# Performance work log

Measured on AMD Instinct MI355X. Metric: run time of the kernel, lower is better.

The kernel has to match this reference:

```python
import jax, jax.numpy as jnp
import numpy as np

NUM_LAYER = 3
LEAKY = 0.8
RES = 0.8  # residual scale in convolution


def spmm(row, col, val, x, n):
    # sparse (n x n) COO @ dense (n x d)
    return jax.ops.segment_sum(val[:, None] * x[col], row, num_segments=n)


def convolution(emb, row, col, val):
    n = emb.shape[0]
    all_e = emb
    acc = emb  # layer-0 term
    for _ in range(NUM_LAYER):
        all_e = spmm(row, col, val, all_e, n) + RES * all_e
        acc = acc + all_e
    return acc / (NUM_LAYER + 1)


def setup_inputs() -> dict:
    key = jax.random.key(0)
    ks = jax.random.split(key, 32)
    B, NU, NQ, NC, DE, DF = 16384, 50000, 20000, 512, 64, 128
    EU, EQ, EK = 1600000, 640000, 16384
    inp = {}
    inp['user_id'] = jax.random.randint(ks[0], (B,), 0, NU)
    inp['question_id'] = jax.random.randint(ks[1], (B,), 0, NQ)
    inp['q_table'] = (jax.random.uniform(ks[2], (NQ, NC)) < 0.05).astype(jnp.float32)
    inp['u_row'] = jax.random.randint(ks[3], (EU,), 0, NU)
    inp['u_col'] = jax.random.randint(ks[4], (EU,), 0, NU)
    inp['u_val'] = jax.random.uniform(ks[5], (EU,)) / 32.0
    inp['e_row'] = jax.random.randint(ks[6], (EQ,), 0, NQ)
    inp['e_col'] = jax.random.randint(ks[7], (EQ,), 0, NQ)
    inp['e_val'] = jax.random.uniform(ks[8], (EQ,)) / 32.0
    inp['k_row'] = jax.random.randint(ks[9], (EK,), 0, NC)
    inp['k_col'] = jax.random.randint(ks[10], (EK,), 0, NC)
    inp['k_val'] = jax.random.uniform(ks[11], (EK,)) / 32.0
    inp['student_emb'] = jax.random.normal(ks[12], (NU, DE)) * 0.1
    inp['exercise_emb'] = jax.random.normal(ks[13], (NQ, DE)) * 0.1
    inp['knowledge_emb'] = jax.random.normal(ks[14], (NC, DE)) * 0.1
    inp['W_s'] = jax.random.normal(ks[15], (DE, DF)) * 0.1
    inp['b_s'] = jnp.zeros((DF,))
    inp['W_e'] = jax.random.normal(ks[16], (DE, DF)) * 0.1
    inp['b_e'] = jnp.zeros((DF,))
    inp['W_k'] = jax.random.normal(ks[17], (DE, DF)) * 0.1
    inp['b_k'] = jnp.zeros((DF,))
    inp['W_d'] = jax.random.normal(ks[18], (DE, 1)) * 0.1
    inp['b_d'] = jnp.zeros((1,))
    inp['M1_w'] = jax.random.normal(ks[19], (NC, 512)) * 0.05
    inp['M1_b'] = jnp.zeros((512,))
    inp['M2_w'] = jax.random.normal(ks[20], (512, 256)) * 0.05
    inp['M2_b'] = jnp.zeros((256,))
    inp['M3_w'] = jax.random.normal(ks[21], (256, 128)) * 0.05
    inp['M3_b'] = jnp.zeros((128,))
    inp['M4_w'] = jax.random.normal(ks[22], (128, 1)) * 0.05
    inp['M4_b'] = jnp.zeros((1,))
    return inp


def reference(user_id, question_id, q_table,
              u_row, u_col, u_val, e_row, e_col, e_val, k_row, k_col, k_val,
              student_emb, exercise_emb, knowledge_emb,
              W_s, b_s, W_e, b_e, W_k, b_k, W_d, b_d,
              M1_w, M1_b, M2_w, M2_b, M3_w, M3_b, M4_w, M4_b):
    cs = convolution(student_emb, u_row, u_col, u_val)    # [NU, DE]
    ce = convolution(exercise_emb, e_row, e_col, e_val)   # [NQ, DE]
    ck = convolution(knowledge_emb, k_row, k_col, k_val)  # [NC, DE]
    bs = cs[user_id]        # [B, DE]
    be = ce[question_id]    # [B, DE]
    sf = jax.nn.leaky_relu(bs @ W_s + b_s, LEAKY)   # [B, DF]
    ef = jax.nn.leaky_relu(be @ W_e + b_e, LEAKY)   # [B, DF]
    kf = jax.nn.leaky_relu(ck @ W_k + b_k, LEAKY)   # [NC, DF]
    disc = jax.nn.sigmoid(be @ W_d + b_d)           # [B, 1]
    state = disc * ((sf - ef) @ kf.T) * q_table[question_id]  # [B, NC]
    h = jnp.tanh(state @ M1_w + M1_b)
    h = jnp.tanh(h @ M2_w + M2_b)
    h = jnp.tanh(h @ M3_w + M3_b)
    return jax.nn.sigmoid(h @ M4_w + M4_b).reshape(-1)  # [B]
```

## Files before the change

### kernel.cpp

```cpp
#include <hip/hip_runtime.h>
#include <hip/hip_bf16.h>
#include <math.h>

#define RESF 0.8f
#define LEAKYF 0.8f
#define BWSH 6
#define BWID 64
#define BSTRIDE 2432
#define BINCH 5120
#define BINR 5

typedef __attribute__((ext_vector_type(8))) short bs8;
typedef __attribute__((ext_vector_type(4))) float f32x4;

__device__ __forceinline__ void gload16(const void* g, void* l) {
  __builtin_amdgcn_global_load_lds((const __attribute__((address_space(1))) void*)g,
                                   (__attribute__((address_space(3))) void*)l, 16, 0, 0);
}

__device__ __forceinline__ float tanh_fast(float x) {
  float t = __expf(2.f * x);
  return 1.f - 2.f * __builtin_amdgcn_rcpf(1.f + t);
}
__device__ __forceinline__ float sigmoid_fast(float x) {
  return __builtin_amdgcn_rcpf(1.f + __expf(-x));
}
__device__ __forceinline__ float bf2f(ushort u) {
  return __uint_as_float((unsigned)u << 16);
}
__device__ __forceinline__ ushort f2bf(float a) {
  __hip_bfloat16 h = __float2bfloat16(a);
  return *(ushort*)&h;
}

__device__ __forceinline__ int edge_row(int e, const int* __restrict__ rU, const int* __restrict__ rE,
                                        const int* __restrict__ rK, int EU, int EQ, int NU, int NQ) {
  if (e < EU) return rU[e];
  if ((e -= EU) < EQ) return NU + rE[e];
  e -= EQ;
  return NU + NQ + rK[e];
}

__device__ __forceinline__ void edge_full(int e,
    const int* __restrict__ rU, const int* __restrict__ cU, const float* __restrict__ vU,
    const int* __restrict__ rE, const int* __restrict__ cE, const float* __restrict__ vE,
    const int* __restrict__ rK, const int* __restrict__ cK, const float* __restrict__ vK,
    int EU, int EQ, int NU, int NQ, int& grow, int& gcol, float& val) {
  if (e < EU) { grow = rU[e]; gcol = cU[e]; val = vU[e]; return; }
  if ((e -= EU) < EQ) { grow = NU + rE[e]; gcol = NU + cE[e]; val = vE[e]; return; }
  e -= EQ;
  grow = NU + NQ + rK[e]; gcol = NU + NQ + cK[e]; val = vK[e];
}

__global__ __launch_bounds__(256) void k_setup(int* __restrict__ gcur, int* __restrict__ flags,
                                               int* __restrict__ nneed, int nbuck, int N_tot) {
  int i = blockIdx.x * 256 + threadIdx.x;
  if (i < nbuck) gcur[i] = i * BSTRIDE;
  if (i < N_tot) flags[i] = 0;
  if (i == 0) nneed[0] = 0;
}

__global__ __launch_bounds__(1024) void k_bin(
    const int* __restrict__ rU, const int* __restrict__ cU, const float* __restrict__ vU,
    const int* __restrict__ rE, const int* __restrict__ cE, const float* __restrict__ vE,
    const int* __restrict__ rK, const int* __restrict__ cK, const float* __restrict__ vK,
    int* __restrict__ gcur, int2* __restrict__ tmp,
    int EU, int EQ, int EK, int NU, int NQ, int nbuck) {
  extern __shared__ int l[];
  int metaN = (2 * nbuck + 3) & ~3;
  int* cnt = l;
  int* dstb = l + nbuck;
  int2* spk = (int2*)(l + metaN);
  ushort* sbk = (ushort*)(spk + BINCH);
  __shared__ int wsum[16];

  int t = threadIdx.x;
  int lane = t & 63, wid = t >> 6;
  for (int i = t; i < nbuck; i += 1024) cnt[i] = 0;
  __syncthreads();

  int E = EU + EQ + EK;
  int lo = blockIdx.x * BINCH;
  int hi = lo + BINCH < E ? lo + BINCH : E;
  int m = hi - lo;

  int2 pk[BINR];
  int bk[BINR];
#pragma unroll
  for (int k = 0; k < BINR; ++k) {
    int e = lo + t + k * 1024;
    bk[k] = -1;
    if (e < hi) {
      int grow, gcol;
      float val;
      edge_full(e, rU, cU, vU, rE, cE, vE, rK, cK, vK, EU, EQ, NU, NQ, grow, gcol, val);
      pk[k].x = ((grow & (BWID - 1)) << 26) | gcol;
      pk[k].y = __float_as_int(val);
      int b = grow >> BWSH;
      bk[k] = b;
      atomicAdd(&cnt[b], 1);
    }
  }
  __syncthreads();

  int carry = 0;
  for (int base = 0; base < nbuck; base += 1024) {
    int i = base + t;
    int x = (i < nbuck) ? cnt[i] : 0;
    int v = x;
#pragma unroll
    for (int d = 1; d < 64; d <<= 1) {
      int y = __shfl_up(v, d);
      if (lane >= d) v += y;
    }
    if (lane == 63) wsum[wid] = v;
    __syncthreads();
    if (t < 16) {
      int w = wsum[t];
#pragma unroll
      for (int d = 1; d < 16; d <<= 1) {
        int y = __shfl_up(w, d);
        if (t >= d) w += y;
      }
      wsum[t] = w;
    }
    __syncthreads();
    int excl = carry + ((wid > 0) ? wsum[wid - 1] : 0) + v - x;
    if (i < nbuck) {
      int gb = x ? atomicAdd(&gcur[i], x) : 0;
      dstb[i] = gb - excl;
      cnt[i] = excl;
    }
    carry += wsum[15];
    __syncthreads();
  }

#pragma unroll
  for (int k = 0; k < BINR; ++k) {
    if (bk[k] >= 0) {
      int p = atomicAdd(&cnt[bk[k]], 1);
      spk[p] = pk[k];
      sbk[p] = (ushort)bk[k];
    }
  }
  __syncthreads();

  for (int i = t; i < m; i += 1024) {
    int b = sbk[i];
    tmp[dstb[b] + i] = spk[i];
  }
}

__global__ __launch_bounds__(1024) void k_scan2(const int* __restrict__ gcur, int* __restrict__ boff, int n) {
  __shared__ int s[16];
  int tid = threadIdx.x;
  int lane = tid & 63, wid = tid >> 6;
  int carry = 0;
  for (int base = 0; base < n; base += 1024) {
    int i = base + tid;
    int x = (i < n) ? (gcur[i] - i * BSTRIDE) : 0;
    int v = x;
#pragma unroll
    for (int d = 1; d < 64; d <<= 1) {
      int t = __shfl_up(v, d);
      if (lane >= d) v += t;
    }
    if (lane == 63) s[wid] = v;
    __syncthreads();
    if (tid < 16) {
      int w = s[tid];
#pragma unroll
      for (int d = 1; d < 16; d <<= 1) {
        int t = __shfl_up(w, d);
        if (tid >= d) w += t;
      }
      s[tid] = w;
    }
    __syncthreads();
    int wofs = (wid > 0) ? s[wid - 1] : 0;
    int total = s[15];
    if (i < n) boff[i] = carry + wofs + v - x;
    carry += total;
    __syncthreads();
  }
  if (tid == 0) boff[n] = carry;
}

__global__ __launch_bounds__(256) void k_sort(const int2* __restrict__ tmp, int2* __restrict__ sorted,
                                              const int* __restrict__ gcur, const int* __restrict__ boff,
                                              int* __restrict__ roff, int N_tot, int E_tot) {
  __shared__ int2 sedge[BSTRIDE];
  __shared__ int cnt[BWID];
  __shared__ int cur[BWID];
  int b = blockIdx.x, t = threadIdx.x;
  int beg = b * BSTRIDE, end = gcur[b];
  int m = end - beg;
  if (m > BSTRIDE) m = BSTRIDE;
  int dst = boff[b];
  if (t < BWID) cnt[t] = 0;
  __syncthreads();
  for (int i = t; i < m; i += 256) {
    int2 pe = tmp[beg + i];
    sedge[i] = pe;
    atomicAdd(&cnt[((unsigned)pe.x) >> 26], 1);
  }
  __syncthreads();
  if (t < BWID) {
    int x = cnt[t];
    int v = x;
#pragma unroll
    for (int d = 1; d < 64; d <<= 1) {
      int y = __shfl_up(v, d);
      if (t >= d) v += y;
    }
    cur[t] = v - x;
    int r = (b << BWSH) + t;
    if (r < N_tot) roff[r] = dst + v - x;
  }
  __syncthreads();
  for (int i = t; i < m; i += 256) {
    int2 pe = sedge[i];
    int rl = ((unsigned)pe.x) >> 26;
    int rank = atomicAdd(&cur[rl], 1);
    sorted[dst + rank] = pe;
  }
  if (b == 0 && t == 0) roff[N_tot] = E_tot;
}

__global__ __launch_bounds__(256) void k_flag(const int* __restrict__ user_id,
                                              const int* __restrict__ question_id,
                                              int* __restrict__ flags, int B, int NU) {
  int i = blockIdx.x * 256 + threadIdx.x;
  if (i < B) {
    flags[user_id[i]] = 1;
    flags[NU + question_id[i]] = 1;
  }
}

__global__ __launch_bounds__(256) void k_compact(const int* __restrict__ flags, int* __restrict__ list,
                                                 int* __restrict__ nneed, int N_tot, int NUQ) {
  int i = blockIdx.x * 256 + threadIdx.x;
  if (i >= N_tot) return;
  if (flags[i] || i >= NUQ) {
    int p = atomicAdd(nneed, 1);
    list[p] = i;
  }
}

__global__ __launch_bounds__(256) void k_init3(ushort* __restrict__ lay0,
                                               const float* __restrict__ embU,
                                               const float* __restrict__ embE,
                                               const float* __restrict__ embK,
                                               int n4U, int n4E, int n4K) {
  int n4 = n4U + n4E + n4K;
  int stride = gridDim.x * 256;
  ushort4* c4 = (ushort4*)lay0;
  for (int i = blockIdx.x * 256 + threadIdx.x; i < n4; i += stride) {
    const float4* src;
    int j = i;
    if (j < n4U) src = (const float4*)embU;
    else if ((j -= n4U) < n4E) src = (const float4*)embE;
    else { j -= n4E; src = (const float4*)embK; }
    float4 v = src[j];
    ushort4 u;
    u.x = f2bf(v.x); u.y = f2bf(v.y); u.z = f2bf(v.z); u.w = f2bf(v.w);
    c4[i] = u;
  }
}

__device__ __forceinline__ void spmm_core(const ushort* __restrict__ curb,
                                          const int2* __restrict__ edges,
                                          int beg, int end, int li, int eh,
                                          float& a0, float& a1, float& a2, float& a3) {
  int lane = (eh << 4) | li;
  for (int base = beg; base < end; base += 64) {
    int rem = end - base;
    int m = rem < 64 ? rem : 64;
    int c = 0, vi = 0;
    if (lane < m) {
      int2 pe = edges[base + lane];
      c = pe.x & 0x3FFFFFF;
      vi = pe.y;
    }
    for (int j = 0; j * 4 < m; j += 4) {
      int s0 = (j + 0) * 4 + eh, s1 = (j + 1) * 4 + eh;
      int s2 = (j + 2) * 4 + eh, s3 = (j + 3) * 4 + eh;
      int cc0 = __shfl(c, s0), cc1 = __shfl(c, s1), cc2 = __shfl(c, s2), cc3 = __shfl(c, s3);
      float vf0 = __int_as_float(__shfl(vi, s0));
      float vf1 = __int_as_float(__shfl(vi, s1));
      float vf2 = __int_as_float(__shfl(vi, s2));
      float vf3 = __int_as_float(__shfl(vi, s3));
      uint2 x0 = *(const uint2*)&curb[(size_t)cc0 * 64 + 4 * li];
      uint2 x1 = *(const uint2*)&curb[(size_t)cc1 * 64 + 4 * li];
      uint2 x2 = *(const uint2*)&curb[(size_t)cc2 * 64 + 4 * li];
      uint2 x3 = *(const uint2*)&curb[(size_t)cc3 * 64 + 4 * li];
      a0 = fmaf(vf0, __uint_as_float(x0.x << 16), a0);
      a1 = fmaf(vf0, __uint_as_float(x0.x & 0xffff0000u), a1);
      a2 = fmaf(vf0, __uint_as_float(x0.y << 16), a2);
      a3 = fmaf(vf0, __uint_as_float(x0.y & 0xffff0000u), a3);
      a0 = fmaf(vf1, __uint_as_float(x1.x << 16), a0);
      a1 = fmaf(vf1, __uint_as_float(x1.x & 0xffff0000u), a1);
      a2 = fmaf(vf1, __uint_as_float(x1.y << 16), a2);
      a3 = fmaf(vf1, __uint_as_float(x1.y & 0xffff0000u), a3);
      a0 = fmaf(vf2, __uint_as_float(x2.x << 16), a0);
      a1 = fmaf(vf2, __uint_as_float(x2.x & 0xffff0000u), a1);
      a2 = fmaf(vf2, __uint_as_float(x2.y << 16), a2);
      a3 = fmaf(vf2, __uint_as_float(x2.y & 0xffff0000u), a3);
      a0 = fmaf(vf3, __uint_as_float(x3.x << 16), a0);
      a1 = fmaf(vf3, __uint_as_float(x3.x & 0xffff0000u), a1);
      a2 = fmaf(vf3, __uint_as_float(x3.y << 16), a2);
      a3 = fmaf(vf3, __uint_as_float(x3.y & 0xffff0000u), a3);
    }
  }
  a0 += __shfl_xor(a0, 16); a0 += __shfl_xor(a0, 32);
  a1 += __shfl_xor(a1, 16); a1 += __shfl_xor(a1, 32);
  a2 += __shfl_xor(a2, 16); a2 += __shfl_xor(a2, 32);
  a3 += __shfl_xor(a3, 16); a3 += __shfl_xor(a3, 32);
}

__global__ __launch_bounds__(256) void k_spmm2(const ushort* __restrict__ curb,
                                               ushort* __restrict__ nxtb,
                                               const int* __restrict__ off,
                                               const int2* __restrict__ edges, int n) {
  int r = blockIdx.x * 4 + (threadIdx.x >> 6);
  if (r >= n) return;
  int lane = threadIdx.x & 63;
  int li = lane & 15, eh = lane >> 4;
  int beg = off[r], end = off[r + 1];
  float a0 = 0.f, a1 = 0.f, a2 = 0.f, a3 = 0.f;
  spmm_core(curb, edges, beg, end, li, eh, a0, a1, a2, a3);
  if (eh == 0) {
    size_t gi = (size_t)r * 64 + 4 * li;
    uint2 cv = *(const uint2*)&curb[gi];
    a0 = fmaf(RESF, __uint_as_float(cv.x << 16), a0);
    a1 = fmaf(RESF, __uint_as_float(cv.x & 0xffff0000u), a1);
    a2 = fmaf(RESF, __uint_as_float(cv.y << 16), a2);
    a3 = fmaf(RESF, __uint_as_float(cv.y & 0xffff0000u), a3);
    uint2 o;
    o.x = ((unsigned)f2bf(a1) << 16) | f2bf(a0);
    o.y = ((unsigned)f2bf(a3) << 16) | f2bf(a2);
    *(uint2*)&nxtb[gi] = o;
  }
}

__global__ __launch_bounds__(256) void k_spmm3(const ushort* __restrict__ curb,
                                               const ushort* __restrict__ lay1,
                                               const float* __restrict__ embU,
                                               const float* __restrict__ embE,
                                               const float* __restrict__ embK,
                                               float* __restrict__ acc,
                                               const int* __restrict__ off,
                                               const int2* __restrict__ edges,
                                               const int* __restrict__ list,
                                               const int* __restrict__ nneed,
                                               int NU, int NQ) {
  int idx = blockIdx.x * 4 + (threadIdx.x >> 6);
  if (idx >= *nneed) return;
  int r = list[idx];
  int lane = threadIdx.x & 63;
  int li = lane & 15, eh = lane >> 4;
  int beg = off[r], end = off[r + 1];
  float a0 = 0.f, a1 = 0.f, a2 = 0.f, a3 = 0.f;
  spmm_core(curb, edges, beg, end, li, eh, a0, a1, a2, a3);
  if (eh == 0) {
    size_t gi = (size_t)r * 64 + 4 * li;
    const float* ep;
    if (r < NU) ep = embU + gi;
    else if (r < NU + NQ) ep = embE + (gi - (size_t)NU * 64);
    else ep = embK + (gi - (size_t)(NU + NQ) * 64);
    float4 e = *(const float4*)ep;
    uint2 l1 = *(const uint2*)&lay1[gi];
    uint2 c2 = *(const uint2*)&curb[gi];
    float c20 = __uint_as_float(c2.x << 16);
    float c21 = __uint_as_float(c2.x & 0xffff0000u);
    float c22 = __uint_as_float(c2.y << 16);
    float c23 = __uint_as_float(c2.y & 0xffff0000u);
    float4 o;
    o.x = e.x + __uint_as_float(l1.x << 16) + c20 + fmaf(RESF, c20, a0);
    o.y = e.y + __uint_as_float(l1.x & 0xffff0000u) + c21 + fmaf(RESF, c21, a1);
    o.z = e.z + __uint_as_float(l1.y << 16) + c22 + fmaf(RESF, c22, a2);
    o.w = e.w + __uint_as_float(l1.y & 0xffff0000u) + c23 + fmaf(RESF, c23, a3);
    *(float4*)&acc[gi] = o;
  }
}

__global__ __launch_bounds__(256) void k_prep(const float* __restrict__ acc_k,
                                              const float* __restrict__ W_k, const float* __restrict__ b_k,
                                              __hip_bfloat16* __restrict__ kfb,
                                              const float* __restrict__ M1_w, __hip_bfloat16* __restrict__ W1t,
                                              const float* __restrict__ M2_w, __hip_bfloat16* __restrict__ W2t,
                                              const float* __restrict__ M3_w, __hip_bfloat16* __restrict__ W3t) {
  int idx = blockIdx.x * 256 + threadIdx.x;
  if (idx < 65536) {
    int d = idx & 127, c = idx >> 7;
    float a = b_k[d];
#pragma unroll 8
    for (int k = 0; k < 64; ++k) a += 0.25f * acc_k[c * 64 + k] * W_k[k * 128 + d];
    float v = a > 0.f ? a : LEAKYF * a;
    kfb[c * 128 + d] = __float2bfloat16(v);
    return;
  }
  int j = idx - 65536;
  if (j < 262144) {
    int n = j >> 9, k = j & 511;
    W1t[n * 512 + k] = __float2bfloat16(M1_w[k * 512 + n]);
    return;
  }
  j -= 262144;
  if (j < 131072) {
    int n = j >> 9, k = j & 511;
    W2t[n * 512 + k] = __float2bfloat16(M2_w[k * 256 + n]);
    return;
  }
  j -= 131072;
  if (j < 32768) {
    int n = j >> 8, k = j & 255;
    W3t[n * 256 + k] = __float2bfloat16(M3_w[k * 128 + n]);
  }
}

__global__ __launch_bounds__(256) void k_diff(
    const int* __restrict__ user_id, const int* __restrict__ question_id,
    const float* __restrict__ acc_u, const float* __restrict__ acc_e,
    const float* __restrict__ W_s, const float* __restrict__ b_s,
    const float* __restrict__ W_e, const float* __restrict__ b_e,
    const float* __restrict__ W_d, const float* __restrict__ b_d,
    __hip_bfloat16* __restrict__ diff, float* __restrict__ disc, int B) {
  __shared__ float bs_l[16 * 64];
  __shared__ float be_l[16 * 64];
  int t = threadIdx.x;
  int row0 = blockIdx.x * 16;
  for (int i = t; i < 16 * 64; i += 256) {
    int r = i >> 6, d = i & 63;
    int gb = row0 + r;
    bs_l[i] = 0.25f * acc_u[(size_t)user_id[gb] * 64 + d];
    be_l[i] = 0.25f * acc_e[(size_t)question_id[gb] * 64 + d];
  }
  __syncthreads();

  int j = t & 127, half = t >> 7;
  float as[8], ae[8];
#pragma unroll
  for (int rr = 0; rr < 8; ++rr) { as[rr] = b_s[j]; ae[rr] = b_e[j]; }
#pragma unroll 4
  for (int k = 0; k < 64; ++k) {
    float ws = W_s[k * 128 + j];
    float we = W_e[k * 128 + j];
#pragma unroll
    for (int rr = 0; rr < 8; ++rr) {
      as[rr] = fmaf(bs_l[(half * 8 + rr) * 64 + k], ws, as[rr]);
      ae[rr] = fmaf(be_l[(half * 8 + rr) * 64 + k], we, ae[rr]);
    }
  }
#pragma unroll
  for (int rr = 0; rr < 8; ++rr) {
    float sfv = as[rr] > 0.f ? as[rr] : LEAKYF * as[rr];
    float efv = ae[rr] > 0.f ? ae[rr] : LEAKYF * ae[rr];
    diff[(size_t)(row0 + half * 8 + rr) * 128 + j] = __float2bfloat16(sfv - efv);
  }
  if (t < 16) {
    float a = b_d[0];
#pragma unroll 8
    for (int k = 0; k < 64; ++k) a = fmaf(be_l[t * 64 + k], W_d[k], a);
    disc[row0 + t] = sigmoid_fast(a);
  }
}

template <int K, int MODE>
__global__ __launch_bounds__(256) void k_gemm(
    const __hip_bfloat16* __restrict__ A, const __hip_bfloat16* __restrict__ Bw,
    __hip_bfloat16* __restrict__ C, int N,
    const float* __restrict__ bias,
    const float* __restrict__ disc, const int* __restrict__ qid,
    const float* __restrict__ q_table) {
  __shared__ __align__(16) short lA[128 * 32];
  __shared__ __align__(16) short lB[128 * 32];
  __shared__ float s_disc[128];
  __shared__ int s_qid[128];
  __shared__ float s_bias[128];

  int t = threadIdx.x;
  int lane = t & 63;
  int w = t >> 6;
  int wr = (w >> 1) * 64, wc = (w & 1) * 64;
  int bm0 = blockIdx.y * 128, bn0 = blockIdx.x * 128;

  if (MODE == 0) {
    if (t < 128) {
      s_disc[t] = disc[bm0 + t];
      s_qid[t] = qid[bm0 + t];
    }
  } else {
    if (t < 128) s_bias[t] = bias[bn0 + t];
  }

  int off0 = t, off1 = 256 + t;
  int rA0 = off0 >> 2, gq0 = (off0 & 3) ^ ((rA0 >> 1) & 3);
  int rA1 = off1 >> 2, gq1 = (off1 & 3) ^ ((rA1 >> 1) & 3);

  const __hip_bfloat16* Ab = A + (size_t)bm0 * K;
  const __hip_bfloat16* Bb = Bw + (size_t)bn0 * K;

  f32x4 acc[4][4] = {};
  int q = lane >> 4, fr = lane & 15;

  for (int k0 = 0; k0 < K; k0 += 32) {
    __syncthreads();
    gload16(Ab + (size_t)rA0 * K + k0 + gq0 * 8, lA + (size_t)off0 * 8);
    gload16(Ab + (size_t)rA1 * K + k0 + gq1 * 8, lA + (size_t)off1 * 8);
    gload16(Bb + (size_t)rA0 * K + k0 + gq0 * 8, lB + (size_t)off0 * 8);
    gload16(Bb + (size_t)rA1 * K + k0 + gq1 * 8, lB + (size_t)off1 * 8);
    __syncthreads();

    bs8 af[4], bf[4];
#pragma unroll
    for (int mi = 0; mi < 4; ++mi) {
      int row = wr + mi * 16 + fr;
      int a16 = row * 4 + (q ^ ((row >> 1) & 3));
      af[mi] = *(const bs8*)&lA[a16 * 8];
    }
#pragma unroll
    for (int ni = 0; ni < 4; ++ni) {
      int col = wc + ni * 16 + fr;
      int b16 = col * 4 + (q ^ ((col >> 1) & 3));
      bf[ni] = *(const bs8*)&lB[b16 * 8];
    }
#pragma unroll
    for (int mi = 0; mi < 4; ++mi)
#pragma unroll
      for (int ni = 0; ni < 4; ++ni)
        acc[mi][ni] = __builtin_amdgcn_mfma_f32_16x16x32_bf16(af[mi], bf[ni], acc[mi][ni], 0, 0, 0);
  }

#pragma unroll
  for (int mi = 0; mi < 4; ++mi) {
    int lr0 = wr + mi * 16 + q * 4;
#pragma unroll
    for (int j = 0; j < 4; ++j) {
      int lr = lr0 + j;
      size_t gr = bm0 + lr;
      float dsc = 0.f;
      size_t qrow = 0;
      if (MODE == 0) {
        dsc = s_disc[lr];
        qrow = (size_t)s_qid[lr] * 512;
      }
#pragma unroll
      for (int ni = 0; ni < 4; ++ni) {
        int lc = wc + ni * 16 + fr;
        int gc = bn0 + lc;
        float v = acc[mi][ni][j];
        if (MODE == 0) {
          v = dsc * v * q_table[qrow + gc];
        } else {
          v = tanh_fast(v + s_bias[lc]);
        }
        C[gr * N + gc] = __float2bfloat16(v);
      }
    }
  }
}

__global__ __launch_bounds__(256) void k_out(const __hip_bfloat16* __restrict__ h3,
                                             const float* __restrict__ M4_w, const float* __restrict__ M4_b,
                                             float* __restrict__ out, int B) {
  __shared__ float sM4[128];
  int t = threadIdx.x;
  if (t < 128) sM4[t] = M4_w[t];
  __syncthreads();
  int w = t >> 6, l = t & 63;
  int row = blockIdx.x * 16 + w * 4 + (l >> 4);
  int k0 = (l & 15) * 8;
  const ushort* hp = (const ushort*)(h3 + (size_t)row * 128 + k0);
  float p = 0.f;
#pragma unroll
  for (int i = 0; i < 8; ++i) {
    float x = __uint_as_float((unsigned)hp[i] << 16);
    p = fmaf(x, sM4[k0 + i], p);
  }
#pragma unroll
  for (int off = 8; off; off >>= 1) p += __shfl_xor(p, off, 16);
  if ((l & 15) == 0 && row < B) out[row] = sigmoid_fast(p + M4_b[0]);
}

static inline int iminh(int a, int b) { return a < b ? a : b; }
static inline size_t rnd4(size_t x) { return (x + 3) & ~(size_t)3; }

extern "C" void kernel_launch(void* const* d_in, const int* in_sizes, int n_in,
                              void* d_out, int out_size, void* d_ws, size_t ws_size,
                              hipStream_t stream) {
  const int* user_id = (const int*)d_in[0];
  const int* question_id = (const int*)d_in[1];
  const float* q_table = (const float*)d_in[2];
  const int* u_row = (const int*)d_in[3];
  const int* u_col = (const int*)d_in[4];
  const float* u_val = (const float*)d_in[5];
  const int* e_row = (const int*)d_in[6];
  const int* e_col = (const int*)d_in[7];
  const float* e_val = (const float*)d_in[8];
  const int* k_row = (const int*)d_in[9];
  const int* k_col = (const int*)d_in[10];
  const float* k_val = (const float*)d_in[11];
  const float* student_emb = (const float*)d_in[12];
  const float* exercise_emb = (const float*)d_in[13];
  const float* knowledge_emb = (const float*)d_in[14];
  const float* W_s = (const float*)d_in[15];
  const float* b_s = (const float*)d_in[16];
  const float* W_e = (const float*)d_in[17];
  const float* b_e = (const float*)d_in[18];
  const float* W_k = (const float*)d_in[19];
  const float* b_k = (const float*)d_in[20];
  const float* W_d = (const float*)d_in[21];
  const float* b_d = (const float*)d_in[22];
  const float* M1_w = (const float*)d_in[23];
  const float* M1_b = (const float*)d_in[24];
  const float* M2_w = (const float*)d_in[25];
  const float* M2_b = (const float*)d_in[26];
  const float* M3_w = (const float*)d_in[27];
  const float* M3_b = (const float*)d_in[28];
  const float* M4_w = (const float*)d_in[29];
  const float* M4_b = (const float*)d_in[30];

  int B = in_sizes[0];
  int NU = in_sizes[12] / 64;
  int NQ = in_sizes[13] / 64;
  int NC = in_sizes[14] / 64;
  int EU = in_sizes[3];
  int EQ = in_sizes[6];
  int EK = in_sizes[9];
  int N_tot = NU + NQ + NC;
  int E_tot = EU + EQ + EK;
  int nbuck = (N_tot + BWID - 1) >> BWSH;

  float* w = (float*)d_ws;
  float* acc = w; w += rnd4((size_t)N_tot * 64);
  __hip_bfloat16* kfb = (__hip_bfloat16*)w; w += rnd4(512 * 128 / 2);
  float* U = w;

  float* acc_u = acc;
  float* acc_e = acc + (size_t)NU * 64;
  float* acc_k = acc + (size_t)(NU + NQ) * 64;

  float* cw = U;
  ushort* lay0 = (ushort*)cw; cw += rnd4((size_t)N_tot * 32);
  ushort* lay1 = (ushort*)cw; cw += rnd4((size_t)N_tot * 32);
  int2* sorted = (int2*)cw;   cw += rnd4((size_t)E_tot * 2);
  int* gcur = (int*)cw;  cw += rnd4(nbuck);
  int* boff = (int*)cw;  cw += rnd4(nbuck + 1);
  int* roff = (int*)cw;  cw += rnd4(N_tot + 1);
  int* flags = (int*)cw; cw += rnd4(N_tot);
  int* list = (int*)cw;  cw += rnd4(N_tot);
  int* nneed = (int*)cw; cw += rnd4(4);
  float* alias0 = cw;
  int2* tmp = (int2*)alias0;
  ushort* lay2 = (ushort*)alias0;
  {
    size_t tmp_f = rnd4((size_t)nbuck * BSTRIDE * 2);
    size_t lay_f = rnd4((size_t)N_tot * 32);
    cw += (tmp_f > lay_f ? tmp_f : lay_f);
  }

  float* mw = U;
  __hip_bfloat16* W1t = (__hip_bfloat16*)mw; mw += rnd4(512 * 512 / 2);
  __hip_bfloat16* W2t = (__hip_bfloat16*)mw; mw += rnd4(256 * 512 / 2);
  __hip_bfloat16* W3t = (__hip_bfloat16*)mw; mw += rnd4(128 * 256 / 2);
  __hip_bfloat16* diff = (__hip_bfloat16*)mw; mw += rnd4((size_t)B * 128 / 2);
  float* disc = mw; mw += rnd4(B);
  __hip_bfloat16* state = (__hip_bfloat16*)mw; mw += rnd4((size_t)B * 512 / 2);
  __hip_bfloat16* h1 = (__hip_bfloat16*)mw;    mw += rnd4((size_t)B * 512 / 2);
  __hip_bfloat16* h2 = state;
  __hip_bfloat16* h3 = diff;

  {
    int gsb = (E_tot + BINCH - 1) / BINCH;
    int metaN = (2 * nbuck + 3) & ~3;
    size_t ldsb = (size_t)metaN * 4 + (size_t)BINCH * 8 + (size_t)BINCH * 2;
    k_setup<<<(N_tot + 255) / 256, 256, 0, stream>>>(gcur, flags, nneed, nbuck, N_tot);
    k_bin<<<gsb, 1024, ldsb, stream>>>(u_row, u_col, u_val, e_row, e_col, e_val,
                                       k_row, k_col, k_val, gcur, tmp,
                                       EU, EQ, EK, NU, NQ, nbuck);
    k_scan2<<<1, 1024, 0, stream>>>(gcur, boff, nbuck);
    k_sort<<<nbuck, 256, 0, stream>>>(tmp, sorted, gcur, boff, roff, N_tot, E_tot);
  }

  k_flag<<<(B + 255) / 256, 256, 0, stream>>>(user_id, question_id, flags, B, NU);
  k_compact<<<(N_tot + 255) / 256, 256, 0, stream>>>(flags, list, nneed, N_tot, NU + NQ);

  {
    int n4 = N_tot * 16;
    int gs = iminh((n4 + 255) / 256, 2048);
    k_init3<<<gs, 256, 0, stream>>>(lay0, student_emb, exercise_emb, knowledge_emb,
                                    NU * 16, NQ * 16, NC * 16);
    k_spmm2<<<(N_tot + 3) / 4, 256, 0, stream>>>(lay0, lay1, roff, sorted, N_tot);
    k_spmm2<<<(N_tot + 3) / 4, 256, 0, stream>>>(lay1, lay2, roff, sorted, N_tot);
    int maxneed = iminh(2 * B + NC, N_tot);
    k_spmm3<<<(maxneed + 3) / 4, 256, 0, stream>>>(lay2, lay1, student_emb, exercise_emb,
                                                   knowledge_emb, acc, roff, sorted,
                                                   list, nneed, NU, NQ);
  }

  k_prep<<<(65536 + 262144 + 131072 + 32768) / 256, 256, 0, stream>>>(
      acc_k, W_k, b_k, kfb, M1_w, W1t, M2_w, W2t, M3_w, W3t);

  k_diff<<<B / 16, 256, 0, stream>>>(user_id, question_id, acc_u, acc_e,
                                     W_s, b_s, W_e, b_e, W_d, b_d, diff, disc, B);

  k_gemm<128, 0><<<dim3(512 / 128, B / 128), 256, 0, stream>>>(
      diff, kfb, state, 512, nullptr, disc, question_id, q_table);
  k_gemm<512, 1><<<dim3(512 / 128, B / 128), 256, 0, stream>>>(
      state, W1t, h1, 512, M1_b, nullptr, nullptr, nullptr);
  k_gemm<512, 1><<<dim3(256 / 128, B / 128), 256, 0, stream>>>(
      h1, W2t, h2, 256, M2_b, nullptr, nullptr, nullptr);
  k_gemm<256, 1><<<dim3(128 / 128, B / 128), 256, 0, stream>>>(
      h2, W3t, h3, 128, M3_b, nullptr, nullptr, nullptr);

  k_out<<<B / 16, 256, 0, stream>>>(h3, M4_w, M4_b, (float*)d_out, B);
}
```

Baseline: 236.0 us.

## Fuse final MLP layer into GEMM, drop compaction kernel, enlarge binning chunks

Three separate changes. The last GEMM gets a MODE 2 epilogue that applies tanh, takes the dot product with M4_w, reduces across lanes and applies the sigmoid, which removes the h3 round trip and the k_out launch. The k_compact pass and its atomic list are replaced by k_spmm3 checking flags directly over all rows, at the cost of launching many more blocks that exit early. k_bin is templated on its chunk size and doubles it to 10240 edges when 160KB of dynamic LDS can be set, halving the number of binning blocks but lowering occupancy.

```diff
diff --git a/kernel.cpp b/kernel.cpp
--- a/kernel.cpp
+++ b/kernel.cpp
@@ -7,8 +7,6 @@
 #define BWSH 6
 #define BWID 64
 #define BSTRIDE 2432
-#define BINCH 5120
-#define BINR 5
 
 typedef __attribute__((ext_vector_type(8))) short bs8;
 typedef __attribute__((ext_vector_type(4))) float f32x4;
@@ -31,14 +29,6 @@
 __device__ __forceinline__ ushort f2bf(float a) {
   __hip_bfloat16 h = __float2bfloat16(a);
   return *(ushort*)&h;
-}
-
-__device__ __forceinline__ int edge_row(int e, const int* __restrict__ rU, const int* __restrict__ rE,
-                                        const int* __restrict__ rK, int EU, int EQ, int NU, int NQ) {
-  if (e < EU) return rU[e];
-  if ((e -= EU) < EQ) return NU + rE[e];
-  e -= EQ;
-  return NU + NQ + rK[e];
 }
 
 __device__ __forceinline__ void edge_full(int e,
@@ -53,19 +43,20 @@
 }
 
 __global__ __launch_bounds__(256) void k_setup(int* __restrict__ gcur, int* __restrict__ flags,
-                                               int* __restrict__ nneed, int nbuck, int N_tot) {
+                                               int nbuck, int N_tot) {
   int i = blockIdx.x * 256 + threadIdx.x;
   if (i < nbuck) gcur[i] = i * BSTRIDE;
   if (i < N_tot) flags[i] = 0;
-  if (i == 0) nneed[0] = 0;
-}
-
+}
+
+template <int BINR>
 __global__ __launch_bounds__(1024) void k_bin(
     const int* __restrict__ rU, const int* __restrict__ cU, const float* __restrict__ vU,
     const int* __restrict__ rE, const int* __restrict__ cE, const float* __restrict__ vE,
     const int* __restrict__ rK, const int* __restrict__ cK, const float* __restrict__ vK,
     int* __restrict__ gcur, int2* __restrict__ tmp,
     int EU, int EQ, int EK, int NU, int NQ, int nbuck) {
+  const int BINCH = BINR * 1024;
   extern __shared__ int l[];
   int metaN = (2 * nbuck + 3) & ~3;
   int* cnt = l;
@@ -229,22 +220,14 @@
 
 __global__ __launch_bounds__(256) void k_flag(const int* __restrict__ user_id,
                                               const int* __restrict__ question_id,
-                                              int* __restrict__ flags, int B, int NU) {
+                                              int* __restrict__ flags, int B, int NU,
+                                              int NUQ, int NC) {
   int i = blockIdx.x * 256 + threadIdx.x;
   if (i < B) {
     flags[user_id[i]] = 1;
     flags[NU + question_id[i]] = 1;
   }
-}
-
-__global__ __launch_bounds__(256) void k_compact(const int* __restrict__ flags, int* __restrict__ list,
-                                                 int* __restrict__ nneed, int N_tot, int NUQ) {
-  int i = blockIdx.x * 256 + threadIdx.x;
-  if (i >= N_tot) return;
-  if (flags[i] || i >= NUQ) {
-    int p = atomicAdd(nneed, 1);
-    list[p] = i;
-  }
+  if (i < NC) flags[NUQ + i] = 1;
 }
 
 __global__ __launch_bounds__(256) void k_init3(ushort* __restrict__ lay0,
@@ -351,12 +334,11 @@
                                                float* __restrict__ acc,
                                                const int* __restrict__ off,
                                                const int2* __restrict__ edges,
-                                               const int* __restrict__ list,
-                                               const int* __restrict__ nneed,
-                                               int NU, int NQ) {
-  int idx = blockIdx.x * 4 + (threadIdx.x >> 6);
-  if (idx >= *nneed) return;
-  int r = list[idx];
+                                               const int* __restrict__ flags,
+                                               int NU, int NQ, int n) {
+  int r = blockIdx.x * 4 + (threadIdx.x >> 6);
+  if (r >= n) return;
+  if (!flags[r]) return;
   int lane = threadIdx.x & 63;
   int li = lane & 15, eh = lane >> 4;
   int beg = off[r], end = off[r + 1];
@@ -472,12 +454,16 @@
     __hip_bfloat16* __restrict__ C, int N,
     const float* __restrict__ bias,
     const float* __restrict__ disc, const int* __restrict__ qid,
-    const float* __restrict__ q_table) {
+    const float* __restrict__ q_table,
+    const float* __restrict__ M4w, const float* __restrict__ M4b,
+    float* __restrict__ outp) {
   __shared__ __align__(16) short lA[128 * 32];
   __shared__ __align__(16) short lB[128 * 32];
   __shared__ float s_disc[128];
   __shared__ int s_qid[128];
   __shared__ float s_bias[128];
+  __shared__ float sM4[128];
+  __shared__ float spart[128][2];
 
   int t = threadIdx.x;
   int lane = t & 63;
@@ -492,6 +478,7 @@
     }
   } else {
     if (t < 128) s_bias[t] = bias[bn0 + t];
+    if (MODE == 2 && t < 128) sM4[t] = M4w[t];
   }
 
   int off0 = t, off1 = 256 + t;
@@ -530,6 +517,30 @@
 #pragma unroll
       for (int ni = 0; ni < 4; ++ni)
         acc[mi][ni] = __builtin_amdgcn_mfma_f32_16x16x32_bf16(af[mi], bf[ni], acc[mi][ni], 0, 0, 0);
+  }
+
+  if (MODE == 2) {
+#pragma unroll
+    for (int mi = 0; mi < 4; ++mi) {
+#pragma unroll
+      for (int j = 0; j < 4; ++j) {
+        int lr = wr + mi * 16 + q * 4 + j;
+        float p = 0.f;
+#pragma unroll
+        for (int ni = 0; ni < 4; ++ni) {
+          int lc = wc + ni * 16 + fr;
+          p += tanh_fast(acc[mi][ni][j] + s_bias[lc]) * sM4[lc];
+        }
+        p += __shfl_xor(p, 1);
+        p += __shfl_xor(p, 2);
+        p += __shfl_xor(p, 4);
+        p += __shfl_xor(p, 8);
+        if (fr == 0) spart[lr][w & 1] = p;
+      }
+    }
+    __syncthreads();
+    if (t < 128) outp[bm0 + t] = sigmoid_fast(spart[t][0] + spart[t][1] + M4b[0]);
+    return;
   }
 
 #pragma unroll
@@ -559,28 +570,6 @@
       }
     }
   }
-}
-
-__global__ __launch_bounds__(256) void k_out(const __hip_bfloat16* __restrict__ h3,
-                                             const float* __restrict__ M4_w, const float* __restrict__ M4_b,
-                                             float* __restrict__ out, int B) {
-  __shared__ float sM4[128];
-  int t = threadIdx.x;
-  if (t < 128) sM4[t] = M4_w[t];
-  __syncthreads();
-  int w = t >> 6, l = t & 63;
-  int row = blockIdx.x * 16 + w * 4 + (l >> 4);
-  int k0 = (l & 15) * 8;
-  const ushort* hp = (const ushort*)(h3 + (size_t)row * 128 + k0);
-  float p = 0.f;
-#pragma unroll
-  for (int i = 0; i < 8; ++i) {
-    float x = __uint_as_float((unsigned)hp[i] << 16);
-    p = fmaf(x, sM4[k0 + i], p);
-  }
-#pragma unroll
-  for (int off = 8; off; off >>= 1) p += __shfl_xor(p, off, 16);
-  if ((l & 15) == 0 && row < B) out[row] = sigmoid_fast(p + M4_b[0]);
 }
 
 static inline int iminh(int a, int b) { return a < b ? a : b; }
@@ -649,8 +638,6 @@
   int* boff = (int*)cw;  cw += rnd4(nbuck + 1);
   int* roff = (int*)cw;  cw += rnd4(N_tot + 1);
   int* flags = (int*)cw; cw += rnd4(N_tot);
-  int* list = (int*)cw;  cw += rnd4(N_tot);
-  int* nneed = (int*)cw; cw += rnd4(4);
   float* alias0 = cw;
   int2* tmp = (int2*)alias0;
   ushort* lay2 = (ushort*)alias0;
@@ -669,22 +656,40 @@
   __hip_bfloat16* state = (__hip_bfloat16*)mw; mw += rnd4((size_t)B * 512 / 2);
   __hip_bfloat16* h1 = (__hip_bfloat16*)mw;    mw += rnd4((size_t)B * 512 / 2);
   __hip_bfloat16* h2 = state;
-  __hip_bfloat16* h3 = diff;
+
+  static int big_ok = -1;
+  if (big_ok < 0) {
+    hipError_t e = hipFuncSetAttribute((const void*)k_bin<10>,
+                                       hipFuncAttributeMaxDynamicSharedMemorySize,
+                                       160 * 1024);
+    big_ok = (e == hipSuccess) ? 1 : 0;
+    (void)hipGetLastError();
+  }
 
   {
-    int gsb = (E_tot + BINCH - 1) / BINCH;
     int metaN = (2 * nbuck + 3) & ~3;
-    size_t ldsb = (size_t)metaN * 4 + (size_t)BINCH * 8 + (size_t)BINCH * 2;
-    k_setup<<<(N_tot + 255) / 256, 256, 0, stream>>>(gcur, flags, nneed, nbuck, N_tot);
-    k_bin<<<gsb, 1024, ldsb, stream>>>(u_row, u_col, u_val, e_row, e_col, e_val,
-                                       k_row, k_col, k_val, gcur, tmp,
-                                       EU, EQ, EK, NU, NQ, nbuck);
+    k_setup<<<(N_tot + 255) / 256, 256, 0, stream>>>(gcur, flags, nbuck, N_tot);
+    if (big_ok) {
+      const int BINCH = 10240;
+      int gsb = (E_tot + BINCH - 1) / BINCH;
+      size_t ldsb = (size_t)metaN * 4 + (size_t)BINCH * 8 + (size_t)BINCH * 2;
+      k_bin<10><<<gsb, 1024, ldsb, stream>>>(u_row, u_col, u_val, e_row, e_col, e_val,
+                                             k_row, k_col, k_val, gcur, tmp,
+                                             EU, EQ, EK, NU, NQ, nbuck);
+    } else {
+      const int BINCH = 5120;
+      int gsb = (E_tot + BINCH - 1) / BINCH;
+      size_t ldsb = (size_t)metaN * 4 + (size_t)BINCH * 8 + (size_t)BINCH * 2;
+      k_bin<5><<<gsb, 1024, ldsb, stream>>>(u_row, u_col, u_val, e_row, e_col, e_val,
+                                            k_row, k_col, k_val, gcur, tmp,
+                                            EU, EQ, EK, NU, NQ, nbuck);
+    }
     k_scan2<<<1, 1024, 0, stream>>>(gcur, boff, nbuck);
     k_sort<<<nbuck, 256, 0, stream>>>(tmp, sorted, gcur, boff, roff, N_tot, E_tot);
   }
 
-  k_flag<<<(B + 255) / 256, 256, 0, stream>>>(user_id, question_id, flags, B, NU);
-  k_compact<<<(N_tot + 255) / 256, 256, 0, stream>>>(flags, list, nneed, N_tot, NU + NQ);
+  k_flag<<<(B + 255) / 256, 256, 0, stream>>>(user_id, question_id, flags, B, NU,
+                                              NU + NQ, NC);
 
   {
     int n4 = N_tot * 16;
@@ -693,10 +698,9 @@
                                     NU * 16, NQ * 16, NC * 16);
     k_spmm2<<<(N_tot + 3) / 4, 256, 0, stream>>>(lay0, lay1, roff, sorted, N_tot);
     k_spmm2<<<(N_tot + 3) / 4, 256, 0, stream>>>(lay1, lay2, roff, sorted, N_tot);
-    int maxneed = iminh(2 * B + NC, N_tot);
-    k_spmm3<<<(maxneed + 3) / 4, 256, 0, stream>>>(lay2, lay1, student_emb, exercise_emb,
-                                                   knowledge_emb, acc, roff, sorted,
-                                                   list, nneed, NU, NQ);
+    k_spmm3<<<(N_tot + 3) / 4, 256, 0, stream>>>(lay2, lay1, student_emb, exercise_emb,
+                                                 knowledge_emb, acc, roff, sorted,
+                                                 flags, NU, NQ, N_tot);
   }
 
   k_prep<<<(65536 + 262144 + 131072 + 32768) / 256, 256, 0, stream>>>(
@@ -706,13 +710,11 @@
                                      W_s, b_s, W_e, b_e, W_d, b_d, diff, disc, B);
 
   k_gemm<128, 0><<<dim3(512 / 128, B / 128), 256, 0, stream>>>(
-      diff, kfb, state, 512, nullptr, disc, question_id, q_table);
+      diff, kfb, state, 512, nullptr, disc, question_id, q_table, nullptr, nullptr, nullptr);
   k_gemm<512, 1><<<dim3(512 / 128, B / 128), 256, 0, stream>>>(
-      state, W1t, h1, 512, M1_b, nullptr, nullptr, nullptr);
+      state, W1t, h1, 512, M1_b, nullptr, nullptr, nullptr, nullptr, nullptr, nullptr);
   k_gemm<512, 1><<<dim3(256 / 128, B / 128), 256, 0, stream>>>(
-      h1, W2t, h2, 256, M2_b, nullptr, nullptr, nullptr);
-  k_gemm<256, 1><<<dim3(128 / 128, B / 128), 256, 0, stream>>>(
-      h2, W3t, h3, 128, M3_b, nullptr, nullptr, nullptr);
-
-  k_out<<<B / 16, 256, 0, stream>>>(h3, M4_w, M4_b, (float*)d_out, B);
-}
+      h1, W2t, h2, 256, M2_b, nullptr, nullptr, nullptr, nullptr, nullptr, nullptr);
+  k_gemm<256, 2><<<dim3(1, B / 128), 256, 0, stream>>>(
+      h2, W3t, nullptr, 128, M3_b, nullptr, nullptr, nullptr, M4_w, M4_b, (float*)d_out);
+}
```

Result: faster. 219.9 us (-6.8%).
